# Performance work log

Hardware: AMD Instinct MI355X
Metric: run time of the kernel (lower is better)

The kernel has to match this reference:

```python
import jax, jax.numpy as jnp
import numpy as np

B, N_TOKENS, E = 64, 512, 512   # batch, document tokens, embedding_dim
MAX_SEQ_LEN = 64                # decode steps


def setup_inputs() -> dict:
    key = jax.random.key(0)
    ks = jax.random.split(key, 11)
    s = 0.05
    return {
        "token_embeddings": jax.random.normal(ks[0], (B, N_TOKENS, 2 * E), jnp.float32),
        "encoded_document": jax.random.normal(ks[1], (B, 2 * E), jnp.float32),
        # LSTMCell params (hidden state is zero every step, so W_hh is dead; biases still add)
        "W_ih": jax.random.normal(ks[2], (4 * E, 2 * E), jnp.float32) * s,
        "b_ih": jax.random.normal(ks[3], (4 * E,), jnp.float32) * s,
        "b_hh": jax.random.normal(ks[4], (4 * E,), jnp.float32) * s,
        # decoder_weights: Linear(E, E)
        "Wd": jax.random.normal(ks[5], (E, E), jnp.float32) * s,
        "bd": jax.random.normal(ks[6], (E,), jnp.float32) * s,
        # encoder_weights: Linear(2E, E)
        "We": jax.random.normal(ks[7], (E, 2 * E), jnp.float32) * s,
        "be": jax.random.normal(ks[8], (E,), jnp.float32) * s,
        # reference: Linear(E, 1)
        "wr": jax.random.normal(ks[9], (1, E), jnp.float32) * s,
        "br": jax.random.normal(ks[10], (1,), jnp.float32) * s,
    }


def reference(token_embeddings, encoded_document, W_ih, b_ih, b_hh, Wd, bd, We, be, wr, br):
    b = token_embeddings.shape[0]
    batch_idx = jnp.arange(b)
    # encoder projection is loop-invariant: hoist it (same math as per-step recompute)
    enc = jnp.einsum('bnd,ed->bne', token_embeddings, We) + be  # [B, N, E]

    def lstm_zero_state(x):
        # PyTorch LSTMCell with default (zero) h, c each call
        gates = x @ W_ih.T + b_ih + b_hh  # [B, 4E]
        i, f, g, o = jnp.split(gates, 4, axis=-1)
        c = jax.nn.sigmoid(i) * jnp.tanh(g)
        return jax.nn.sigmoid(o) * jnp.tanh(c)

    def step(dec_in, _):
        hx = lstm_zero_state(dec_in)              # [B, E]
        q = hx @ Wd.T + bd                        # [B, E]
        comp = jnp.tanh(q[:, None, :] + enc)      # [B, N, E]
        scores = jnp.einsum('bne,e->bn', comp, wr[0]) + br[0]  # [B, N]
        logp = jax.nn.log_softmax(scores, axis=1)
        idx = jnp.argmax(logp, axis=1)            # [B]
        nxt = token_embeddings[batch_idx, idx]    # [B, 2E]
        return nxt, (logp, idx)

    _, (probs, idxs) = jax.lax.scan(step, encoded_document, None, length=MAX_SEQ_LEN)
    overall_probabilities = jnp.transpose(probs, (1, 0, 2))  # [B, MAX_SEQ_LEN, N]
    peak_indices = idxs.T                                     # [B, MAX_SEQ_LEN]
    return overall_probabilities, peak_indices
```

## Files before the change

### kernel.cpp

```cpp
#include <hip/hip_runtime.h>


#define DEV __device__ __forceinline__

DEV float sigm(float x) { return __fdividef(1.0f, 1.0f + __expf(-x)); }
DEV float tanh_fast(float x) {
  float e = __expf(2.0f * x);
  return 1.0f - __fdividef(2.0f, e + 1.0f);
}

DEV unsigned long long pack_score(float s, int n) {
  unsigned u = __float_as_uint(s);
  unsigned key = (u & 0x80000000u) ? ~u : (u | 0x80000000u);
  return ((unsigned long long)key << 32) | (unsigned)(511 - n);
}
DEV float unpack_score(unsigned long long p) {
  unsigned key = (unsigned)(p >> 32);
  unsigned u = (key & 0x80000000u) ? (key & 0x7fffffffu) : ~key;
  return __uint_as_float(u);
}
DEV int unpack_idx(unsigned long long p) { return 511 - (int)(p & 0xffffu); }

#define FMA4(acc, xv, wv)                                                      \
  acc = fmaf((xv).x, (wv).x, acc); acc = fmaf((xv).y, (wv).y, acc);            \
  acc = fmaf((xv).z, (wv).z, acc); acc = fmaf((xv).w, (wv).w, acc)

__global__ __launch_bounds__(256) void kenc(const float* __restrict__ A,
                                            const float* __restrict__ Bm,
                                            const float* __restrict__ bias,
                                            float* __restrict__ C) {
  __shared__ float a_s[16][132];
  __shared__ float b_s[16][132];
  const int t = threadIdx.x;
  const int row = t >> 1;
  const int kq = (t & 1) * 8;
  const float* Arow = A + (blockIdx.x * 128 + row) * 1024 + kq;
  const float* Brow = Bm + (blockIdx.y * 128 + row) * 1024 + kq;
  const int tx = t & 15, ty = t >> 4;
  float acc[8][8] = {};
  for (int k0 = 0; k0 < 1024; k0 += 16) {
    float4 av0 = *(const float4*)(Arow + k0);
    float4 av1 = *(const float4*)(Arow + k0 + 4);
    float4 bv0 = *(const float4*)(Brow + k0);
    float4 bv1 = *(const float4*)(Brow + k0 + 4);
    __syncthreads();
    a_s[kq+0][row]=av0.x; a_s[kq+1][row]=av0.y; a_s[kq+2][row]=av0.z; a_s[kq+3][row]=av0.w;
    a_s[kq+4][row]=av1.x; a_s[kq+5][row]=av1.y; a_s[kq+6][row]=av1.z; a_s[kq+7][row]=av1.w;
    b_s[kq+0][row]=bv0.x; b_s[kq+1][row]=bv0.y; b_s[kq+2][row]=bv0.z; b_s[kq+3][row]=bv0.w;
    b_s[kq+4][row]=bv1.x; b_s[kq+5][row]=bv1.y; b_s[kq+6][row]=bv1.z; b_s[kq+7][row]=bv1.w;
    __syncthreads();
    #pragma unroll
    for (int k = 0; k < 16; ++k) {
      float a[8], b[8];
      *(float4*)(a)   = *(const float4*)&a_s[k][ty*4];
      *(float4*)(a+4) = *(const float4*)&a_s[k][64 + ty*4];
      *(float4*)(b)   = *(const float4*)&b_s[k][tx*4];
      *(float4*)(b+4) = *(const float4*)&b_s[k][64 + tx*4];
      #pragma unroll
      for (int i = 0; i < 8; ++i)
        #pragma unroll
        for (int j = 0; j < 8; ++j)
          acc[i][j] = fmaf(a[i], b[j], acc[i][j]);
    }
  }
  const int mb = blockIdx.x * 128;
  const int eb = blockIdx.y * 128;
  float4 bv0 = *(const float4*)&bias[eb + tx*4];
  float4 bv1 = *(const float4*)&bias[eb + 64 + tx*4];
  #pragma unroll
  for (int i = 0; i < 8; ++i) {
    const int r = mb + ((i < 4) ? (ty*4 + i) : (64 + ty*4 + (i - 4)));
    float* orow = C + r * 512 + eb;
    float4 o0, o1;
    o0.x=acc[i][0]+bv0.x; o0.y=acc[i][1]+bv0.y; o0.z=acc[i][2]+bv0.z; o0.w=acc[i][3]+bv0.w;
    o1.x=acc[i][4]+bv1.x; o1.y=acc[i][5]+bv1.y; o1.z=acc[i][6]+bv1.z; o1.w=acc[i][7]+bv1.w;
    *(float4*)(orow + tx*4) = o0;
    *(float4*)(orow + 64 + tx*4) = o1;
  }
}

__global__ __launch_bounds__(256) void kstep(
    const float* __restrict__ TE, const float* __restrict__ encd,
    const float* __restrict__ W_ih, const float* __restrict__ b_ih,
    const float* __restrict__ b_hh, const float* __restrict__ scores,
    const unsigned long long* __restrict__ mprev,
    unsigned long long* __restrict__ mcur,
    float* __restrict__ hx, float* __restrict__ out_logp,
    float* __restrict__ out_idx, int step) {
  __shared__ int   idx_s[64];
  __shared__ float mx_s[64];
  __shared__ float wsum_s[4];
  __shared__ float part_s[4][64][6];
  const int g = blockIdx.x;
  const int t = threadIdx.x;
  const int lane = t & 63;
  const int wu = __builtin_amdgcn_readfirstlane(t >> 6);

  if (g == 0 && t < 64) mcur[t] = 0ULL;

  if (step > 0 && t < 64) {
    unsigned long long p = mprev[t];
    idx_s[t] = unpack_idx(p);
    mx_s[t]  = unpack_score(p);
  }
  __syncthreads();

  if (step > 0 && g < 64) {
    const float* srow = scores + g * 512;
    const float mx = mx_s[g];
    float ssum = __expf(srow[t] - mx) + __expf(srow[t + 256] - mx);
    #pragma unroll
    for (int m = 1; m <= 32; m <<= 1) ssum += __shfl_xor(ssum, m);
    if (lane == 0) wsum_s[wu] = ssum;
  }
  __syncthreads();
  if (step > 0 && g < 64) {
    const float* srow = scores + g * 512;
    const float lse = mx_s[g] + __logf(wsum_s[0] + wsum_s[1] + wsum_s[2] + wsum_s[3]);
    float* orow = out_logp + (g * 64 + (step - 1)) * 512;
    orow[t]       = srow[t]       - lse;
    orow[t + 256] = srow[t + 256] - lse;
    if (t == 0) out_idx[g * 64 + (step - 1)] = (float)idx_s[g];
  }

  const int k0 = 2 * g, k1 = 2 * g + 1;
  const int dbase = wu * 256;
  const float* p0 = W_ih + (k0        ) * 1024 + dbase;
  const float* p1 = W_ih + (k1        ) * 1024 + dbase;
  const float* p2 = W_ih + (1024 + k0) * 1024 + dbase;
  const float* p3 = W_ih + (1024 + k1) * 1024 + dbase;
  const float* p4 = W_ih + (1536 + k0) * 1024 + dbase;
  const float* p5 = W_ih + (1536 + k1) * 1024 + dbase;
  const float* xr = (step == 0) ? (encd + lane * 1024 + dbase)
                                : (TE + (lane * 512 + idx_s[lane]) * 1024 + dbase);
  float a0=0, a1=0, a2=0, a3=0, a4=0, a5=0;
  #pragma unroll 4
  for (int d = 0; d < 256; d += 4) {
    float4 xv = *(const float4*)(xr + d);
    float4 v0 = *(const float4*)(p0 + d);
    float4 v1 = *(const float4*)(p1 + d);
    float4 v2 = *(const float4*)(p2 + d);
    float4 v3 = *(const float4*)(p3 + d);
    float4 v4 = *(const float4*)(p4 + d);
    float4 v5 = *(const float4*)(p5 + d);
    FMA4(a0, xv, v0); FMA4(a1, xv, v1); FMA4(a2, xv, v2);
    FMA4(a3, xv, v3); FMA4(a4, xv, v4); FMA4(a5, xv, v5);
  }
  part_s[wu][lane][0]=a0; part_s[wu][lane][1]=a1; part_s[wu][lane][2]=a2;
  part_s[wu][lane][3]=a3; part_s[wu][lane][4]=a4; part_s[wu][lane][5]=a5;
  __syncthreads();

  if (t < 64) {
    float s0=0, s1=0, s2=0, s3=0, s4=0, s5=0;
    #pragma unroll
    for (int u = 0; u < 4; ++u) {
      s0 += part_s[u][t][0]; s1 += part_s[u][t][1]; s2 += part_s[u][t][2];
      s3 += part_s[u][t][3]; s4 += part_s[u][t][4]; s5 += part_s[u][t][5];
    }
    const float gi0 = s0 + b_ih[k0] + b_hh[k0];
    const float gi1 = s1 + b_ih[k1] + b_hh[k1];
    const float gg0 = s2 + b_ih[1024 + k0] + b_hh[1024 + k0];
    const float gg1 = s3 + b_ih[1024 + k1] + b_hh[1024 + k1];
    const float go0 = s4 + b_ih[1536 + k0] + b_hh[1536 + k0];
    const float go1 = s5 + b_ih[1536 + k1] + b_hh[1536 + k1];
    const float c0 = sigm(gi0) * tanh_fast(gg0);
    const float c1 = sigm(gi1) * tanh_fast(gg1);
    hx[t * 512 + k0] = sigm(go0) * tanh_fast(c0);
    hx[t * 512 + k1] = sigm(go1) * tanh_fast(c1);
  }
}

__global__ __launch_bounds__(256) void kq(const float* __restrict__ hx,
                                          const float* __restrict__ Wd,
                                          const float* __restrict__ bd,
                                          float* __restrict__ q) {
  __shared__ float part_s[4][64][2];
  const int g = blockIdx.x;
  const int t = threadIdx.x, lane = t & 63;
  const int wu = __builtin_amdgcn_readfirstlane(t >> 6);
  const int dbase = wu * 128;
  const int e0 = g * 2;
  const float* w0 = Wd + (e0 + 0) * 512 + dbase;
  const float* w1 = Wd + (e0 + 1) * 512 + dbase;
  const float* xr = hx + lane * 512 + dbase;
  float a0=0, a1=0;
  #pragma unroll 8
  for (int d = 0; d < 128; d += 4) {
    float4 xv = *(const float4*)(xr + d);
    float4 v0 = *(const float4*)(w0 + d);
    float4 v1 = *(const float4*)(w1 + d);
    FMA4(a0, xv, v0); FMA4(a1, xv, v1);
  }
  part_s[wu][lane][0]=a0; part_s[wu][lane][1]=a1;
  __syncthreads();
  if (t < 64) {
    float2 r;
    r.x = part_s[0][t][0]+part_s[1][t][0]+part_s[2][t][0]+part_s[3][t][0] + bd[e0+0];
    r.y = part_s[0][t][1]+part_s[1][t][1]+part_s[2][t][1]+part_s[3][t][1] + bd[e0+1];
    *(float2*)(q + t * 512 + e0) = r;
  }
}

__global__ __launch_bounds__(256) void kscore(const float* __restrict__ enc,
                                              const float* __restrict__ q,
                                              const float* __restrict__ wr,
                                              const float* __restrict__ br,
                                              float* __restrict__ scores,
                                              unsigned long long* __restrict__ mtop) {
  __shared__ unsigned long long lmax;
  const int bid = blockIdx.x;
  const int b = bid >> 4, c = bid & 15;
  const int t = threadIdx.x, lane = t & 63, wu = t >> 6;
  const int le = lane & 15, nl = lane >> 4;
  if (t == 0) lmax = 0ULL;
  const float C2 = 2.8853900817779268f;
  float4 wv[8], cq[8];
  const float* qrow = q + b * 512 + le * 4;
  const float* wrp  = wr + le * 4;
  float swv = 0.0f;
  #pragma unroll
  for (int j = 0; j < 8; ++j) {
    wv[j] = *(const float4*)(wrp + 64 * j);
    swv += wv[j].x + wv[j].y + wv[j].z + wv[j].w;
    float4 qv = *(const float4*)(qrow + 64 * j);
    cq[j].x = C2*qv.x; cq[j].y = C2*qv.y; cq[j].z = C2*qv.z; cq[j].w = C2*qv.w;
  }
  swv += __shfl_xor(swv, 1); swv += __shfl_xor(swv, 2);
  swv += __shfl_xor(swv, 4); swv += __shfl_xor(swv, 8);
  const float brv = br[0];
  __syncthreads();
  #pragma unroll
  for (int i = 0; i < 2; ++i) {
    const int n = c * 32 + wu * 8 + i * 4 + nl;
    const float* erow = enc + (b * 512 + n) * 512 + le * 4;
    float acc = 0.0f;
    #pragma unroll
    for (int j = 0; j < 8; ++j) {
      float4 ev = *(const float4*)(erow + 64 * j);
      acc = fmaf(wv[j].x, __fdividef(1.0f, __builtin_exp2f(fmaf(C2, ev.x, cq[j].x)) + 1.0f), acc);
      acc = fmaf(wv[j].y, __fdividef(1.0f, __builtin_exp2f(fmaf(C2, ev.y, cq[j].y)) + 1.0f), acc);
      acc = fmaf(wv[j].z, __fdividef(1.0f, __builtin_exp2f(fmaf(C2, ev.z, cq[j].z)) + 1.0f), acc);
      acc = fmaf(wv[j].w, __fdividef(1.0f, __builtin_exp2f(fmaf(C2, ev.w, cq[j].w)) + 1.0f), acc);
    }
    acc += __shfl_xor(acc, 1); acc += __shfl_xor(acc, 2);
    acc += __shfl_xor(acc, 4); acc += __shfl_xor(acc, 8);
    if (le == 0) {
      const float sc = swv - 2.0f * acc + brv;
      scores[b * 512 + n] = sc;
      atomicMax(&lmax, pack_score(sc, n));
    }
  }
  __syncthreads();
  if (t == 0) atomicMax(&mtop[b], lmax);
}

__global__ __launch_bounds__(256) void kfin(const float* __restrict__ scores,
                                            const unsigned long long* __restrict__ mtop,
                                            float* __restrict__ out_logp,
                                            float* __restrict__ out_idx) {
  __shared__ float sw[4];
  const int b = blockIdx.x, t = threadIdx.x, lane = t & 63, w = t >> 6;
  const float* srow = scores + b * 512;
  const float s1 = srow[t], s2 = srow[t + 256];
  const unsigned long long p = mtop[b];
  const float mx = unpack_score(p);
  float ssum = __expf(s1 - mx) + __expf(s2 - mx);
  #pragma unroll
  for (int m = 1; m <= 32; m <<= 1) ssum += __shfl_xor(ssum, m);
  if (lane == 0) sw[w] = ssum;
  __syncthreads();
  const float lse = mx + __logf(sw[0] + sw[1] + sw[2] + sw[3]);
  float* orow = out_logp + (b * 64 + 63) * 512;
  orow[t]       = s1 - lse;
  orow[t + 256] = s2 - lse;
  if (t == 0) out_idx[b * 64 + 63] = (float)unpack_idx(p);
}

extern "C" void kernel_launch(void* const* d_in, const int* in_sizes, int n_in,
                              void* d_out, int out_size, void* d_ws, size_t ws_size,
                              hipStream_t stream) {
  const float* TE   = (const float*)d_in[0];
  const float* encd = (const float*)d_in[1];
  const float* W_ih = (const float*)d_in[2];
  const float* b_ih = (const float*)d_in[3];
  const float* b_hh = (const float*)d_in[4];
  const float* Wd   = (const float*)d_in[5];
  const float* bd   = (const float*)d_in[6];
  const float* We   = (const float*)d_in[7];
  const float* be   = (const float*)d_in[8];
  const float* wr   = (const float*)d_in[9];
  const float* br   = (const float*)d_in[10];

  float* out     = (float*)d_out;
  float* out_idx = out + 64 * 64 * 512;

  float* enc    = (float*)d_ws;
  float* scores = enc + 16777216;
  float* hx     = scores + 32768;
  float* q      = hx + 32768;
  unsigned long long* mbuf0 = (unsigned long long*)(q + 32768);
  unsigned long long* mbuf1 = mbuf0 + 64;

  kenc<<<dim3(256, 4), 256, 0, stream>>>(TE, We, be, enc);
  for (int t = 0; t < 64; ++t) {
    unsigned long long* mprev = (t & 1) ? mbuf0 : mbuf1;
    unsigned long long* mcur  = (t & 1) ? mbuf1 : mbuf0;
    kstep<<<256, 256, 0, stream>>>(TE, encd, W_ih, b_ih, b_hh, scores, mprev,
                                   mcur, hx, out, out_idx, t);
    kq<<<256, 256, 0, stream>>>(hx, Wd, bd, q);
    kscore<<<1024, 256, 0, stream>>>(enc, q, wr, br, scores, mcur);
  }
  kfin<<<64, 256, 0, stream>>>(scores, mbuf1, out, out_idx);
}
```

Measured before the change: 3.111 ms.

## Fuse per-step LSTM, query and score kernels with in-kernel grid flags

Merges the three per-decode-step kernels (LSTM gates, query projection, attention scores) into one 1024-block kernel. Stages are ordered with global atomic counters used as grid-wide flag barriers instead of separate launches. Per-step max buffers now get a separate slot for every step, zeroed once with a memset, which removes the double-buffer reset. This cuts kernel launches and inter-kernel gaps, but relies on all 1024 blocks being resident at once and adds spin-wait cost.

```diff
diff --git a/kernel.cpp b/kernel.cpp
--- a/kernel.cpp
+++ b/kernel.cpp
@@ -79,179 +79,190 @@
   }
 }
 
-__global__ __launch_bounds__(256) void kstep(
+DEV void flag_signal(unsigned* p) {
+  __hip_atomic_fetch_add(p, 1u, __ATOMIC_RELEASE, __HIP_MEMORY_SCOPE_AGENT);
+}
+DEV void flag_wait(unsigned* p, unsigned target) {
+  while (__hip_atomic_load(p, __ATOMIC_RELAXED, __HIP_MEMORY_SCOPE_AGENT) < target)
+    __builtin_amdgcn_s_sleep(8);
+  __builtin_amdgcn_fence(__ATOMIC_ACQUIRE, "agent");
+}
+
+__global__ __launch_bounds__(256, 4) void kdec(
     const float* __restrict__ TE, const float* __restrict__ encd,
     const float* __restrict__ W_ih, const float* __restrict__ b_ih,
-    const float* __restrict__ b_hh, const float* __restrict__ scores,
-    const unsigned long long* __restrict__ mprev,
-    unsigned long long* __restrict__ mcur,
-    float* __restrict__ hx, float* __restrict__ out_logp,
-    float* __restrict__ out_idx, int step) {
+    const float* __restrict__ b_hh, const float* __restrict__ Wd,
+    const float* __restrict__ bd, const float* __restrict__ wr,
+    const float* __restrict__ br, const float* __restrict__ enc,
+    float* __restrict__ scores, float* __restrict__ hx, float* __restrict__ q,
+    unsigned long long* __restrict__ mall, unsigned* __restrict__ flags,
+    float* __restrict__ out_logp, float* __restrict__ out_idx, int step) {
   __shared__ int   idx_s[64];
   __shared__ float mx_s[64];
   __shared__ float wsum_s[4];
   __shared__ float part_s[4][64][6];
+  __shared__ float partq_s[4][64][2];
+  __shared__ unsigned long long lmax;
   const int g = blockIdx.x;
   const int t = threadIdx.x;
   const int lane = t & 63;
   const int wu = __builtin_amdgcn_readfirstlane(t >> 6);
-
-  if (g == 0 && t < 64) mcur[t] = 0ULL;
-
-  if (step > 0 && t < 64) {
-    unsigned long long p = mprev[t];
-    idx_s[t] = unpack_idx(p);
-    mx_s[t]  = unpack_score(p);
-  }
+  unsigned* hx_done = flags + step * 2;
+  unsigned* q_done  = hx_done + 1;
+  const unsigned long long* mprev = mall + (step - 1) * 64;
+  unsigned long long* mcur = mall + step * 64;
+  if (t == 0) lmax = 0ULL;
+
+  if (g < 256) {
+    if (step > 0 && t < 64) {
+      unsigned long long p = mprev[t];
+      idx_s[t] = unpack_idx(p);
+      mx_s[t]  = unpack_score(p);
+    }
+    __syncthreads();
+
+    if (step > 0 && g < 64) {
+      const float* srow = scores + g * 512;
+      const float mx = mx_s[g];
+      float ssum = __expf(srow[t] - mx) + __expf(srow[t + 256] - mx);
+      #pragma unroll
+      for (int m = 1; m <= 32; m <<= 1) ssum += __shfl_xor(ssum, m);
+      if (lane == 0) wsum_s[wu] = ssum;
+    }
+    __syncthreads();
+    if (step > 0 && g < 64) {
+      const float* srow = scores + g * 512;
+      const float lse = mx_s[g] + __logf(wsum_s[0] + wsum_s[1] + wsum_s[2] + wsum_s[3]);
+      float* orow = out_logp + (g * 64 + (step - 1)) * 512;
+      orow[t]       = srow[t]       - lse;
+      orow[t + 256] = srow[t + 256] - lse;
+      if (t == 0) out_idx[g * 64 + (step - 1)] = (float)idx_s[g];
+    }
+
+    {
+      const int k0 = 2 * g, k1 = 2 * g + 1;
+      const int dbase = wu * 256;
+      const float* p0 = W_ih + (k0        ) * 1024 + dbase;
+      const float* p1 = W_ih + (k1        ) * 1024 + dbase;
+      const float* p2 = W_ih + (1024 + k0) * 1024 + dbase;
+      const float* p3 = W_ih + (1024 + k1) * 1024 + dbase;
+      const float* p4 = W_ih + (1536 + k0) * 1024 + dbase;
+      const float* p5 = W_ih + (1536 + k1) * 1024 + dbase;
+      const float* xr = (step == 0) ? (encd + lane * 1024 + dbase)
+                                    : (TE + (lane * 512 + idx_s[lane]) * 1024 + dbase);
+      float a0=0, a1=0, a2=0, a3=0, a4=0, a5=0;
+      #pragma unroll 4
+      for (int d = 0; d < 256; d += 4) {
+        float4 xv = *(const float4*)(xr + d);
+        float4 v0 = *(const float4*)(p0 + d);
+        float4 v1 = *(const float4*)(p1 + d);
+        float4 v2 = *(const float4*)(p2 + d);
+        float4 v3 = *(const float4*)(p3 + d);
+        float4 v4 = *(const float4*)(p4 + d);
+        float4 v5 = *(const float4*)(p5 + d);
+        FMA4(a0, xv, v0); FMA4(a1, xv, v1); FMA4(a2, xv, v2);
+        FMA4(a3, xv, v3); FMA4(a4, xv, v4); FMA4(a5, xv, v5);
+      }
+      part_s[wu][lane][0]=a0; part_s[wu][lane][1]=a1; part_s[wu][lane][2]=a2;
+      part_s[wu][lane][3]=a3; part_s[wu][lane][4]=a4; part_s[wu][lane][5]=a5;
+      __syncthreads();
+      if (t < 64) {
+        float s0=0, s1=0, s2=0, s3=0, s4=0, s5=0;
+        #pragma unroll
+        for (int u = 0; u < 4; ++u) {
+          s0 += part_s[u][t][0]; s1 += part_s[u][t][1]; s2 += part_s[u][t][2];
+          s3 += part_s[u][t][3]; s4 += part_s[u][t][4]; s5 += part_s[u][t][5];
+        }
+        const float gi0 = s0 + b_ih[k0] + b_hh[k0];
+        const float gi1 = s1 + b_ih[k1] + b_hh[k1];
+        const float gg0 = s2 + b_ih[1024 + k0] + b_hh[1024 + k0];
+        const float gg1 = s3 + b_ih[1024 + k1] + b_hh[1024 + k1];
+        const float go0 = s4 + b_ih[1536 + k0] + b_hh[1536 + k0];
+        const float go1 = s5 + b_ih[1536 + k1] + b_hh[1536 + k1];
+        const float c0 = sigm(gi0) * tanh_fast(gg0);
+        const float c1 = sigm(gi1) * tanh_fast(gg1);
+        hx[t * 512 + k0] = sigm(go0) * tanh_fast(c0);
+        hx[t * 512 + k1] = sigm(go1) * tanh_fast(c1);
+      }
+    }
+    __syncthreads();
+    if (t == 0) {
+      flag_signal(hx_done);
+      flag_wait(hx_done, 256u);
+    }
+    __syncthreads();
+
+    {
+      const int dbase = wu * 128;
+      const int e0 = g * 2;
+      const float* w0 = Wd + (e0 + 0) * 512 + dbase;
+      const float* w1 = Wd + (e0 + 1) * 512 + dbase;
+      const float* xr = hx + lane * 512 + dbase;
+      float a0=0, a1=0;
+      #pragma unroll 8
+      for (int d = 0; d < 128; d += 4) {
+        float4 xv = *(const float4*)(xr + d);
+        float4 v0 = *(const float4*)(w0 + d);
+        float4 v1 = *(const float4*)(w1 + d);
+        FMA4(a0, xv, v0); FMA4(a1, xv, v1);
+      }
+      partq_s[wu][lane][0]=a0; partq_s[wu][lane][1]=a1;
+      __syncthreads();
+      if (t < 64) {
+        float2 r;
+        r.x = partq_s[0][t][0]+partq_s[1][t][0]+partq_s[2][t][0]+partq_s[3][t][0] + bd[e0+0];
+        r.y = partq_s[0][t][1]+partq_s[1][t][1]+partq_s[2][t][1]+partq_s[3][t][1] + bd[e0+1];
+        *(float2*)(q + t * 512 + e0) = r;
+      }
+    }
+    __syncthreads();
+    if (t == 0) flag_signal(q_done);
+  }
+
+  if (t == 0) flag_wait(q_done, 256u);
   __syncthreads();
-
-  if (step > 0 && g < 64) {
-    const float* srow = scores + g * 512;
-    const float mx = mx_s[g];
-    float ssum = __expf(srow[t] - mx) + __expf(srow[t + 256] - mx);
-    #pragma unroll
-    for (int m = 1; m <= 32; m <<= 1) ssum += __shfl_xor(ssum, m);
-    if (lane == 0) wsum_s[wu] = ssum;
-  }
-  __syncthreads();
-  if (step > 0 && g < 64) {
-    const float* srow = scores + g * 512;
-    const float lse = mx_s[g] + __logf(wsum_s[0] + wsum_s[1] + wsum_s[2] + wsum_s[3]);
-    float* orow = out_logp + (g * 64 + (step - 1)) * 512;
-    orow[t]       = srow[t]       - lse;
-    orow[t + 256] = srow[t + 256] - lse;
-    if (t == 0) out_idx[g * 64 + (step - 1)] = (float)idx_s[g];
-  }
-
-  const int k0 = 2 * g, k1 = 2 * g + 1;
-  const int dbase = wu * 256;
-  const float* p0 = W_ih + (k0        ) * 1024 + dbase;
-  const float* p1 = W_ih + (k1        ) * 1024 + dbase;
-  const float* p2 = W_ih + (1024 + k0) * 1024 + dbase;
-  const float* p3 = W_ih + (1024 + k1) * 1024 + dbase;
-  const float* p4 = W_ih + (1536 + k0) * 1024 + dbase;
-  const float* p5 = W_ih + (1536 + k1) * 1024 + dbase;
-  const float* xr = (step == 0) ? (encd + lane * 1024 + dbase)
-                                : (TE + (lane * 512 + idx_s[lane]) * 1024 + dbase);
-  float a0=0, a1=0, a2=0, a3=0, a4=0, a5=0;
-  #pragma unroll 4
-  for (int d = 0; d < 256; d += 4) {
-    float4 xv = *(const float4*)(xr + d);
-    float4 v0 = *(const float4*)(p0 + d);
-    float4 v1 = *(const float4*)(p1 + d);
-    float4 v2 = *(const float4*)(p2 + d);
-    float4 v3 = *(const float4*)(p3 + d);
-    float4 v4 = *(const float4*)(p4 + d);
-    float4 v5 = *(const float4*)(p5 + d);
-    FMA4(a0, xv, v0); FMA4(a1, xv, v1); FMA4(a2, xv, v2);
-    FMA4(a3, xv, v3); FMA4(a4, xv, v4); FMA4(a5, xv, v5);
-  }
-  part_s[wu][lane][0]=a0; part_s[wu][lane][1]=a1; part_s[wu][lane][2]=a2;
-  part_s[wu][lane][3]=a3; part_s[wu][lane][4]=a4; part_s[wu][lane][5]=a5;
-  __syncthreads();
-
-  if (t < 64) {
-    float s0=0, s1=0, s2=0, s3=0, s4=0, s5=0;
-    #pragma unroll
-    for (int u = 0; u < 4; ++u) {
-      s0 += part_s[u][t][0]; s1 += part_s[u][t][1]; s2 += part_s[u][t][2];
-      s3 += part_s[u][t][3]; s4 += part_s[u][t][4]; s5 += part_s[u][t][5];
-    }
-    const float gi0 = s0 + b_ih[k0] + b_hh[k0];
-    const float gi1 = s1 + b_ih[k1] + b_hh[k1];
-    const float gg0 = s2 + b_ih[1024 + k0] + b_hh[1024 + k0];
-    const float gg1 = s3 + b_ih[1024 + k1] + b_hh[1024 + k1];
-    const float go0 = s4 + b_ih[1536 + k0] + b_hh[1536 + k0];
-    const float go1 = s5 + b_ih[1536 + k1] + b_hh[1536 + k1];
-    const float c0 = sigm(gi0) * tanh_fast(gg0);
-    const float c1 = sigm(gi1) * tanh_fast(gg1);
-    hx[t * 512 + k0] = sigm(go0) * tanh_fast(c0);
-    hx[t * 512 + k1] = sigm(go1) * tanh_fast(c1);
-  }
-}
-
-__global__ __launch_bounds__(256) void kq(const float* __restrict__ hx,
-                                          const float* __restrict__ Wd,
-                                          const float* __restrict__ bd,
-                                          float* __restrict__ q) {
-  __shared__ float part_s[4][64][2];
-  const int g = blockIdx.x;
-  const int t = threadIdx.x, lane = t & 63;
-  const int wu = __builtin_amdgcn_readfirstlane(t >> 6);
-  const int dbase = wu * 128;
-  const int e0 = g * 2;
-  const float* w0 = Wd + (e0 + 0) * 512 + dbase;
-  const float* w1 = Wd + (e0 + 1) * 512 + dbase;
-  const float* xr = hx + lane * 512 + dbase;
-  float a0=0, a1=0;
-  #pragma unroll 8
-  for (int d = 0; d < 128; d += 4) {
-    float4 xv = *(const float4*)(xr + d);
-    float4 v0 = *(const float4*)(w0 + d);
-    float4 v1 = *(const float4*)(w1 + d);
-    FMA4(a0, xv, v0); FMA4(a1, xv, v1);
-  }
-  part_s[wu][lane][0]=a0; part_s[wu][lane][1]=a1;
-  __syncthreads();
-  if (t < 64) {
-    float2 r;
-    r.x = part_s[0][t][0]+part_s[1][t][0]+part_s[2][t][0]+part_s[3][t][0] + bd[e0+0];
-    r.y = part_s[0][t][1]+part_s[1][t][1]+part_s[2][t][1]+part_s[3][t][1] + bd[e0+1];
-    *(float2*)(q + t * 512 + e0) = r;
-  }
-}
-
-__global__ __launch_bounds__(256) void kscore(const float* __restrict__ enc,
-                                              const float* __restrict__ q,
-                                              const float* __restrict__ wr,
-                                              const float* __restrict__ br,
-                                              float* __restrict__ scores,
-                                              unsigned long long* __restrict__ mtop) {
-  __shared__ unsigned long long lmax;
-  const int bid = blockIdx.x;
-  const int b = bid >> 4, c = bid & 15;
-  const int t = threadIdx.x, lane = t & 63, wu = t >> 6;
-  const int le = lane & 15, nl = lane >> 4;
-  if (t == 0) lmax = 0ULL;
-  const float C2 = 2.8853900817779268f;
-  float4 wv[8], cq[8];
-  const float* qrow = q + b * 512 + le * 4;
-  const float* wrp  = wr + le * 4;
-  float swv = 0.0f;
-  #pragma unroll
-  for (int j = 0; j < 8; ++j) {
-    wv[j] = *(const float4*)(wrp + 64 * j);
-    swv += wv[j].x + wv[j].y + wv[j].z + wv[j].w;
-    float4 qv = *(const float4*)(qrow + 64 * j);
-    cq[j].x = C2*qv.x; cq[j].y = C2*qv.y; cq[j].z = C2*qv.z; cq[j].w = C2*qv.w;
-  }
-  swv += __shfl_xor(swv, 1); swv += __shfl_xor(swv, 2);
-  swv += __shfl_xor(swv, 4); swv += __shfl_xor(swv, 8);
-  const float brv = br[0];
-  __syncthreads();
-  #pragma unroll
-  for (int i = 0; i < 2; ++i) {
-    const int n = c * 32 + wu * 8 + i * 4 + nl;
-    const float* erow = enc + (b * 512 + n) * 512 + le * 4;
-    float acc = 0.0f;
+  {
+    const int b = g >> 4, c = g & 15;
+    const int le = lane & 15, nl = lane >> 4;
+    const float C2 = 2.8853900817779268f;
+    float4 wv[8], cq[8];
+    const float* qrow = q + b * 512 + le * 4;
+    const float* wrp  = wr + le * 4;
+    float swv = 0.0f;
     #pragma unroll
     for (int j = 0; j < 8; ++j) {
-      float4 ev = *(const float4*)(erow + 64 * j);
-      acc = fmaf(wv[j].x, __fdividef(1.0f, __builtin_exp2f(fmaf(C2, ev.x, cq[j].x)) + 1.0f), acc);
-      acc = fmaf(wv[j].y, __fdividef(1.0f, __builtin_exp2f(fmaf(C2, ev.y, cq[j].y)) + 1.0f), acc);
-      acc = fmaf(wv[j].z, __fdividef(1.0f, __builtin_exp2f(fmaf(C2, ev.z, cq[j].z)) + 1.0f), acc);
-      acc = fmaf(wv[j].w, __fdividef(1.0f, __builtin_exp2f(fmaf(C2, ev.w, cq[j].w)) + 1.0f), acc);
-    }
-    acc += __shfl_xor(acc, 1); acc += __shfl_xor(acc, 2);
-    acc += __shfl_xor(acc, 4); acc += __shfl_xor(acc, 8);
-    if (le == 0) {
-      const float sc = swv - 2.0f * acc + brv;
-      scores[b * 512 + n] = sc;
-      atomicMax(&lmax, pack_score(sc, n));
+      wv[j] = *(const float4*)(wrp + 64 * j);
+      swv += wv[j].x + wv[j].y + wv[j].z + wv[j].w;
+      float4 qv = *(const float4*)(qrow + 64 * j);
+      cq[j].x = C2*qv.x; cq[j].y = C2*qv.y; cq[j].z = C2*qv.z; cq[j].w = C2*qv.w;
+    }
+    swv += __shfl_xor(swv, 1); swv += __shfl_xor(swv, 2);
+    swv += __shfl_xor(swv, 4); swv += __shfl_xor(swv, 8);
+    const float brv = br[0];
+    #pragma unroll
+    for (int i = 0; i < 2; ++i) {
+      const int n = c * 32 + wu * 8 + i * 4 + nl;
+      const float* erow = enc + (b * 512 + n) * 512 + le * 4;
+      float acc = 0.0f;
+      #pragma unroll
+      for (int j = 0; j < 8; ++j) {
+        float4 ev = *(const float4*)(erow + 64 * j);
+        acc = fmaf(wv[j].x, __fdividef(1.0f, __builtin_exp2f(fmaf(C2, ev.x, cq[j].x)) + 1.0f), acc);
+        acc = fmaf(wv[j].y, __fdividef(1.0f, __builtin_exp2f(fmaf(C2, ev.y, cq[j].y)) + 1.0f), acc);
+        acc = fmaf(wv[j].z, __fdividef(1.0f, __builtin_exp2f(fmaf(C2, ev.z, cq[j].z)) + 1.0f), acc);
+        acc = fmaf(wv[j].w, __fdividef(1.0f, __builtin_exp2f(fmaf(C2, ev.w, cq[j].w)) + 1.0f), acc);
+      }
+      acc += __shfl_xor(acc, 1); acc += __shfl_xor(acc, 2);
+      acc += __shfl_xor(acc, 4); acc += __shfl_xor(acc, 8);
+      if (le == 0) {
+        const float sc = swv - 2.0f * acc + brv;
+        scores[b * 512 + n] = sc;
+        atomicMax(&lmax, pack_score(sc, n));
+      }
     }
   }
   __syncthreads();
-  if (t == 0) atomicMax(&mtop[b], lmax);
+  if (t == 0) atomicMax(&mcur[g >> 4], lmax);
 }
 
 __global__ __launch_bounds__(256) void kfin(const float* __restrict__ scores,
@@ -298,17 +309,15 @@
   float* scores = enc + 16777216;
   float* hx     = scores + 32768;
   float* q      = hx + 32768;
-  unsigned long long* mbuf0 = (unsigned long long*)(q + 32768);
-  unsigned long long* mbuf1 = mbuf0 + 64;
-
+  unsigned long long* mall = (unsigned long long*)(q + 32768);
+  unsigned* flags = (unsigned*)(mall + 64 * 64);
+
+  hipMemsetAsync(mall, 0, 64 * 64 * 8 + 64 * 2 * 4, stream);
   kenc<<<dim3(256, 4), 256, 0, stream>>>(TE, We, be, enc);
   for (int t = 0; t < 64; ++t) {
-    unsigned long long* mprev = (t & 1) ? mbuf0 : mbuf1;
-    unsigned long long* mcur  = (t & 1) ? mbuf1 : mbuf0;
-    kstep<<<256, 256, 0, stream>>>(TE, encd, W_ih, b_ih, b_hh, scores, mprev,
-                                   mcur, hx, out, out_idx, t);
-    kq<<<256, 256, 0, stream>>>(hx, Wd, bd, q);
-    kscore<<<1024, 256, 0, stream>>>(enc, q, wr, br, scores, mcur);
-  }
-  kfin<<<64, 256, 0, stream>>>(scores, mbuf1, out, out_idx);
-}
+    kdec<<<1024, 256, 0, stream>>>(TE, encd, W_ih, b_ih, b_hh, Wd, bd, wr, br,
+                                   enc, scores, hx, q, mall, flags, out,
+                                   out_idx, t);
+  }
+  kfin<<<64, 256, 0, stream>>>(scores, mall + 63 * 64, out, out_idx);
+}
```

New measurement: 6.526 ms. 2.1x slower.

## Fuse decoder query projection into score kernel, recomputing q per block

Applied to the files above, without the earlier changes.

Merges the separate q-projection kernel into the attention-score kernel. Each block loads its batch's hx into shared memory, computes the full 512-wide q row from Wd, and then scores 256 tokens. This removes one launch per step and the global round trip for q. In exchange the grid drops from 1024 to 128 blocks, the full Wd matrix is read redundantly by every block with per-thread strided rows, and fewer CUs share the dominant tanh/score work.

```diff
diff --git a/kernel.cpp b/kernel.cpp
--- a/kernel.cpp
+++ b/kernel.cpp
@@ -170,68 +170,59 @@
   }
 }
 
-__global__ __launch_bounds__(256) void kq(const float* __restrict__ hx,
-                                          const float* __restrict__ Wd,
-                                          const float* __restrict__ bd,
-                                          float* __restrict__ q) {
-  __shared__ float part_s[4][64][2];
-  const int g = blockIdx.x;
-  const int t = threadIdx.x, lane = t & 63;
-  const int wu = __builtin_amdgcn_readfirstlane(t >> 6);
-  const int dbase = wu * 128;
-  const int e0 = g * 2;
-  const float* w0 = Wd + (e0 + 0) * 512 + dbase;
-  const float* w1 = Wd + (e0 + 1) * 512 + dbase;
-  const float* xr = hx + lane * 512 + dbase;
-  float a0=0, a1=0;
-  #pragma unroll 8
-  for (int d = 0; d < 128; d += 4) {
-    float4 xv = *(const float4*)(xr + d);
-    float4 v0 = *(const float4*)(w0 + d);
-    float4 v1 = *(const float4*)(w1 + d);
-    FMA4(a0, xv, v0); FMA4(a1, xv, v1);
-  }
-  part_s[wu][lane][0]=a0; part_s[wu][lane][1]=a1;
-  __syncthreads();
-  if (t < 64) {
-    float2 r;
-    r.x = part_s[0][t][0]+part_s[1][t][0]+part_s[2][t][0]+part_s[3][t][0] + bd[e0+0];
-    r.y = part_s[0][t][1]+part_s[1][t][1]+part_s[2][t][1]+part_s[3][t][1] + bd[e0+1];
-    *(float2*)(q + t * 512 + e0) = r;
-  }
-}
-
-__global__ __launch_bounds__(256) void kscore(const float* __restrict__ enc,
-                                              const float* __restrict__ q,
-                                              const float* __restrict__ wr,
-                                              const float* __restrict__ br,
-                                              float* __restrict__ scores,
-                                              unsigned long long* __restrict__ mtop) {
+__global__ __launch_bounds__(256) void kqs(const float* __restrict__ enc,
+                                           const float* __restrict__ hx,
+                                           const float* __restrict__ Wd,
+                                           const float* __restrict__ bd,
+                                           const float* __restrict__ wr,
+                                           const float* __restrict__ br,
+                                           float* __restrict__ scores,
+                                           unsigned long long* __restrict__ mtop) {
+  __shared__ float hx_s[512];
+  __shared__ float q_s[512];
   __shared__ unsigned long long lmax;
   const int bid = blockIdx.x;
-  const int b = bid >> 4, c = bid & 15;
+  const int b = bid >> 1, c = bid & 1;
   const int t = threadIdx.x, lane = t & 63, wu = t >> 6;
+  if (t == 0) lmax = 0ULL;
+  hx_s[t]       = hx[b * 512 + t];
+  hx_s[256 + t] = hx[b * 512 + 256 + t];
+  __syncthreads();
+
+  {
+    const float* w0 = Wd + (2 * t) * 512;
+    const float* w1 = w0 + 512;
+    float a0 = 0.0f, a1 = 0.0f;
+    #pragma unroll 8
+    for (int d = 0; d < 512; d += 4) {
+      float4 xv = *(const float4*)&hx_s[d];
+      float4 v0 = *(const float4*)(w0 + d);
+      float4 v1 = *(const float4*)(w1 + d);
+      FMA4(a0, xv, v0); FMA4(a1, xv, v1);
+    }
+    q_s[2 * t]     = a0 + bd[2 * t];
+    q_s[2 * t + 1] = a1 + bd[2 * t + 1];
+  }
+  __syncthreads();
+
   const int le = lane & 15, nl = lane >> 4;
-  if (t == 0) lmax = 0ULL;
   const float C2 = 2.8853900817779268f;
   float4 wv[8], cq[8];
-  const float* qrow = q + b * 512 + le * 4;
-  const float* wrp  = wr + le * 4;
+  const float* wrp = wr + le * 4;
   float swv = 0.0f;
   #pragma unroll
   for (int j = 0; j < 8; ++j) {
     wv[j] = *(const float4*)(wrp + 64 * j);
     swv += wv[j].x + wv[j].y + wv[j].z + wv[j].w;
-    float4 qv = *(const float4*)(qrow + 64 * j);
+    float4 qv = *(const float4*)&q_s[le * 4 + 64 * j];
     cq[j].x = C2*qv.x; cq[j].y = C2*qv.y; cq[j].z = C2*qv.z; cq[j].w = C2*qv.w;
   }
   swv += __shfl_xor(swv, 1); swv += __shfl_xor(swv, 2);
   swv += __shfl_xor(swv, 4); swv += __shfl_xor(swv, 8);
   const float brv = br[0];
-  __syncthreads();
-  #pragma unroll
-  for (int i = 0; i < 2; ++i) {
-    const int n = c * 32 + wu * 8 + i * 4 + nl;
+  #pragma unroll 2
+  for (int i = 0; i < 16; ++i) {
+    const int n = c * 256 + wu * 64 + i * 4 + nl;
     const float* erow = enc + (b * 512 + n) * 512 + le * 4;
     float acc = 0.0f;
     #pragma unroll
@@ -297,8 +288,7 @@
   float* enc    = (float*)d_ws;
   float* scores = enc + 16777216;
   float* hx     = scores + 32768;
-  float* q      = hx + 32768;
-  unsigned long long* mbuf0 = (unsigned long long*)(q + 32768);
+  unsigned long long* mbuf0 = (unsigned long long*)(hx + 32768);
   unsigned long long* mbuf1 = mbuf0 + 64;
 
   kenc<<<dim3(256, 4), 256, 0, stream>>>(TE, We, be, enc);
@@ -307,8 +297,7 @@
     unsigned long long* mcur  = (t & 1) ? mbuf1 : mbuf0;
     kstep<<<256, 256, 0, stream>>>(TE, encd, W_ih, b_ih, b_hh, scores, mprev,
                                    mcur, hx, out, out_idx, t);
-    kq<<<256, 256, 0, stream>>>(hx, Wd, bd, q);
-    kscore<<<1024, 256, 0, stream>>>(enc, q, wr, br, scores, mcur);
+    kqs<<<128, 256, 0, stream>>>(enc, hx, Wd, bd, wr, br, scores, mcur);
   }
   kfin<<<64, 256, 0, stream>>>(scores, mbuf1, out, out_idx);
 }
```

Result: slower. 6.004 ms (+93.0%).
